# Optimization experiments

Measured on AMD Instinct MI355X. Metric: run time of the kernel, lower is better.

## Reference

```python
import jax, jax.numpy as jnp
import numpy as np

NEG_SLOPE = 0.2  # PyG GATv2Conv default negative_slope


def gatv2_layer(x, src, dst, Wl, bl, Wr, br, att, bias, concat):
    """GATv2Conv (PyG semantics): message j->i, softmax over incoming edges of i."""
    N = x.shape[0]
    H, C = att.shape
    xl = (x @ Wl + bl).reshape(N, H, C)  # source-side transform
    xr = (x @ Wr + br).reshape(N, H, C)  # target-side transform
    msg = xl[src]                                   # [E,H,C] gathered source feats
    e = jax.nn.leaky_relu(msg + xr[dst], NEG_SLOPE)  # [E,H,C]
    score = jnp.einsum('ehc,hc->eh', e, att)        # [E,H]
    # segment softmax over destination node (every node has a self loop -> no empty segment)
    smax = jax.ops.segment_max(score, dst, num_segments=N)
    ex = jnp.exp(score - smax[dst])
    denom = jax.ops.segment_sum(ex, dst, num_segments=N)
    alpha = ex / denom[dst]                         # [E,H]
    out = jax.ops.segment_sum(alpha[:, :, None] * msg, dst, num_segments=N)  # [N,H,C]
    out = out.reshape(N, H * C) if concat else out.mean(axis=1)
    return out + bias


def setup_inputs():
    key = jax.random.key(0)
    ks = jax.random.split(key, 16)
    N, E = 50000, 800000
    D_in, Hd, H, D_out = 128, 32, 4, 64
    HC = Hd * H  # 128
    s = 0.05
    return {
        'x': jax.random.normal(ks[0], (N, D_in), jnp.float32),
        'edge_index': jax.random.randint(ks[1], (2, E), 0, N, dtype=jnp.int32),
        # layer 1: GATv2Conv(D_in, Hd, heads=H)
        'Wl1': jax.random.normal(ks[2], (D_in, HC), jnp.float32) * s,
        'bl1': jnp.zeros((HC,), jnp.float32),
        'Wr1': jax.random.normal(ks[3], (D_in, HC), jnp.float32) * s,
        'br1': jnp.zeros((HC,), jnp.float32),
        'att1': jax.random.normal(ks[4], (H, Hd), jnp.float32) * s,
        'bias1': jnp.zeros((HC,), jnp.float32),
        # layer 2: GATv2Conv(HC, D_out, heads=1, concat=False)
        'Wl2': jax.random.normal(ks[5], (HC, D_out), jnp.float32) * s,
        'bl2': jnp.zeros((D_out,), jnp.float32),
        'Wr2': jax.random.normal(ks[6], (HC, D_out), jnp.float32) * s,
        'br2': jnp.zeros((D_out,), jnp.float32),
        'att2': jax.random.normal(ks[7], (1, D_out), jnp.float32) * s,
        'bias2': jnp.zeros((D_out,), jnp.float32),
    }


def reference(x, edge_index, Wl1, bl1, Wr1, br1, att1, bias1,
              Wl2, bl2, Wr2, br2, att2, bias2):
    N = x.shape[0]
    loops = jnp.arange(N, dtype=edge_index.dtype)  # add_self_loops=True (PyG default)
    src = jnp.concatenate([edge_index[0], loops])
    dst = jnp.concatenate([edge_index[1], loops])
    h = gatv2_layer(x, src, dst, Wl1, bl1, Wr1, br1, att1, bias1, concat=True)
    h = jax.nn.relu(h)
    out = gatv2_layer(h, src, dst, Wl2, bl2, Wr2, br2, att2, bias2, concat=False)
    return out
```

## Files before the change

kernel.cpp:

```cpp
#include <hip/hip_runtime.h>
#include <hip/hip_bf16.h>
#include <math.h>


#define NSLOPE 0.2f
#define L2E 1.4426950408889634f
#define BKT 64
#define POISON 0xAAAAAAAAu

typedef __attribute__((ext_vector_type(8))) short short8;
typedef __attribute__((ext_vector_type(4))) float f32x4;
typedef _Float16 h16x2 __attribute__((ext_vector_type(2)));

__device__ inline unsigned short f2bf(float f) {
  unsigned int u = __float_as_uint(f);
  u += 0x7fff + ((u >> 16) & 1);
  return (unsigned short)(u >> 16);
}
__device__ inline float bf2f(unsigned short h) {
  return __uint_as_float(((unsigned int)h) << 16);
}

__device__ inline float merge2(float qa, float qb, int m, int lane) {
  bool hi = (lane & m) != 0;
  float sel = hi ? qb : qa;
  float oth = hi ? qa : qb;
  return sel + __shfl_xor(oth, m);
}

template <typename AT>
__device__ __forceinline__ void gemm_body(const AT* __restrict__ A,
    const float* __restrict__ Wl, const float* __restrict__ Wr,
    const float* __restrict__ bl, const float* __restrict__ br,
    _Float16* __restrict__ xl, _Float16* __restrict__ xr, int C, int M,
    int mblk, int g, unsigned short* smem) {
  unsigned short* sBh = smem;
  unsigned short* sBl = smem + 8192;
  int t = threadIdx.x;
  for (int s = t; s < 1024; s += 256) {
    int lane = s & 63;
    int kt = (s >> 6) & 3;
    int tn = s >> 8;
    int n = g * 64 + tn * 16 + (lane & 15);
    int k0 = kt * 32 + ((lane >> 4) * 8);
    const float* W = (n < C) ? (Wl + n) : (Wr + (n - C));
    int base = ((tn * 4 + kt) * 64 + lane) * 8;
#pragma unroll
    for (int j = 0; j < 8; j++) {
      float v = W[(size_t)(k0 + j) * C];
      unsigned short hi = f2bf(v);
      sBh[base + j] = hi;
      sBl[base + j] = f2bf(v - bf2f(hi));
    }
  }
  __syncthreads();
  int w = t >> 6, l = t & 63;
  int m_base = mblk * 128 + w * 32;
  int mrow = l & 15;
  int kq = l >> 4;
  f32x4 acc[2][4];
#pragma unroll
  for (int mt = 0; mt < 2; mt++)
#pragma unroll
    for (int tn = 0; tn < 4; tn++) acc[mt][tn] = (f32x4){0.f, 0.f, 0.f, 0.f};

#pragma unroll
  for (int kt = 0; kt < 4; kt++) {
    short8 ah[2], al[2];
#pragma unroll
    for (int mt = 0; mt < 2; mt++) {
      int m = m_base + mt * 16 + mrow;
      m = (m < M) ? m : (M - 1);
      const AT* pa = A + (size_t)m * 128 + kt * 32 + kq * 8;
      float f[8];
      if constexpr (sizeof(AT) == 4) {
        float4 v0 = *(const float4*)pa;
        float4 v1 = *(const float4*)(pa + 4);
        f[0] = v0.x; f[1] = v0.y; f[2] = v0.z; f[3] = v0.w;
        f[4] = v1.x; f[5] = v1.y; f[6] = v1.z; f[7] = v1.w;
      } else {
        h16x2 h0 = *(const h16x2*)(pa + 0);
        h16x2 h1 = *(const h16x2*)(pa + 2);
        h16x2 h2 = *(const h16x2*)(pa + 4);
        h16x2 h3 = *(const h16x2*)(pa + 6);
        f[0] = (float)h0.x; f[1] = (float)h0.y; f[2] = (float)h1.x; f[3] = (float)h1.y;
        f[4] = (float)h2.x; f[5] = (float)h2.y; f[6] = (float)h3.x; f[7] = (float)h3.y;
      }
#pragma unroll
      for (int j = 0; j < 8; j++) {
        unsigned short hi = f2bf(f[j]);
        ah[mt][j] = (short)hi;
        al[mt][j] = (short)f2bf(f[j] - bf2f(hi));
      }
    }
#pragma unroll
    for (int tn = 0; tn < 4; tn++) {
      int off = ((tn * 4 + kt) * 64 + l) * 8;
      short8 bh = *(const short8*)(sBh + off);
      short8 blo = *(const short8*)(sBl + off);
#pragma unroll
      for (int mt = 0; mt < 2; mt++) {
        acc[mt][tn] = __builtin_amdgcn_mfma_f32_16x16x32_bf16(ah[mt], bh, acc[mt][tn], 0, 0, 0);
        acc[mt][tn] = __builtin_amdgcn_mfma_f32_16x16x32_bf16(ah[mt], blo, acc[mt][tn], 0, 0, 0);
        acc[mt][tn] = __builtin_amdgcn_mfma_f32_16x16x32_bf16(al[mt], bh, acc[mt][tn], 0, 0, 0);
      }
    }
  }
  __syncthreads();
  _Float16* stg = (_Float16*)(smem + w * 2304);
#pragma unroll
  for (int tn = 0; tn < 4; tn++) {
    int col = tn * 16 + mrow;
    int bn = g * 64 + col;
    float bias = (bn < C) ? bl[bn] : br[bn - C];
#pragma unroll
    for (int mt = 0; mt < 2; mt++) {
#pragma unroll
      for (int r = 0; r < 4; r++) {
        int row = mt * 16 + kq * 4 + r;
        stg[row * 72 + col] = (_Float16)(acc[mt][tn][r] + bias);
      }
    }
  }
  int gcol = g * 64;
  _Float16* outp = (gcol < C) ? (xl + gcol) : (xr + (gcol - C));
  int row8 = l >> 3, sub = l & 7;
#pragma unroll
  for (int ig = 0; ig < 4; ig++) {
    int row = ig * 8 + row8;
    int m = m_base + row;
    if (m < M) {
      float4 v = *(const float4*)(stg + row * 72 + sub * 8);
      *(float4*)(outp + (size_t)m * C + sub * 8) = v;
    }
  }
}


__global__ __launch_bounds__(256) void fat1_kernel(
    const int* __restrict__ srcv, const int* __restrict__ dstv,
    unsigned int* __restrict__ counts, unsigned short* __restrict__ bucket, int E,
    const float* __restrict__ A,
    const float* __restrict__ Wl, const float* __restrict__ Wr,
    const float* __restrict__ bl, const float* __restrict__ br,
    _Float16* __restrict__ xl, _Float16* __restrict__ xr, int M,
    int countBlocks, int P) {
  __shared__ unsigned short smem[16384];
  int b = blockIdx.x;
  bool isCount = ((b % P) == (P - 1)) && (b / P < countBlocks);
  if (isCount) {
    int cb = b / P;
    int base = cb * 2048 + threadIdx.x;
    int d[8], s[8];
    unsigned r[8];
#pragma unroll
    for (int u = 0; u < 8; u++) {
      int idx = base + u * 256;
      d[u] = (idx < E) ? dstv[idx] : -1;
      s[u] = (idx < E) ? srcv[idx] : 0;
    }
#pragma unroll
    for (int u = 0; u < 8; u++)
      if (d[u] >= 0) r[u] = atomicAdd(&counts[d[u]], 1u) - POISON;
#pragma unroll
    for (int u = 0; u < 8; u++)
      if (d[u] >= 0 && r[u] < BKT) bucket[(size_t)d[u] * BKT + r[u]] = (unsigned short)s[u];
  } else {
    int nbelow = b / P;
    nbelow = nbelow < countBlocks ? nbelow : countBlocks;
    int bid = b - nbelow;
    gemm_body<float>(A, Wl, Wr, bl, br, xl, xr, 128, M, bid >> 2, bid & 3, smem);
  }
}

__global__ __launch_bounds__(256) void gemm2_kernel(const _Float16* __restrict__ A,
    const float* __restrict__ Wl, const float* __restrict__ Wr,
    const float* __restrict__ bl, const float* __restrict__ br,
    _Float16* __restrict__ xl, _Float16* __restrict__ xr, int M) {
  __shared__ unsigned short smem[16384];
  gemm_body<_Float16>(A, Wl, Wr, bl, br, xl, xr, 64, M, blockIdx.x >> 1, blockIdx.x & 1, smem);
}


__device__ inline h16x2 leaky_pk(h16x2 s) {
  h16x2 s2 = s * (h16x2){(_Float16)NSLOPE, (_Float16)NSLOPE};
  return __builtin_elementwise_max(s, s2);
}

__global__ __launch_bounds__(256) void edge1_kernel(
    const _Float16* __restrict__ xl, const _Float16* __restrict__ xr,
    const float* __restrict__ att, const float* __restrict__ bias,
    const unsigned int* __restrict__ counts, const unsigned short* __restrict__ bucket,
    _Float16* __restrict__ h, int N) {
  int node = blockIdx.x * 4 + (threadIdx.x >> 6);
  if (node >= N) return;
  int lane = threadIdx.x & 63;
  int c = lane * 2;
  h16x2 xri = *(const h16x2*)(xr + (size_t)node * 128 + c);
  float2 atf = *(const float2*)(att + c);
  h16x2 at = {(_Float16)(atf.x * L2E), (_Float16)(atf.y * L2E)};
  unsigned dg = counts[node] - POISON;
  int deg = __builtin_amdgcn_readfirstlane((int)(dg < BKT ? dg : BKT));
  const uint4* brow = (const uint4*)(bucket + (size_t)node * BKT);
  int base16 = lane & 48;
  float l, a0, a1;
  {
    h16x2 ms = *(const h16x2*)(xl + (size_t)node * 128 + c);
    h16x2 lk = leaky_pk(ms + xri);
    float q = __builtin_amdgcn_fdot2(lk, at, 0.f, false);
    q += __shfl_xor(q, 1);
    q += __shfl_xor(q, 2);
    q += __shfl_xor(q, 4);
    q += __shfl_xor(q, 8);
    float p = exp2f(q);
    l = p; a0 = p * (float)ms.x; a1 = p * (float)ms.y;
  }
  for (int e = 0; e < deg; e += 8) {
    uint4 pk = brow[e >> 3];
    int j[8];
    j[0] = __builtin_amdgcn_readfirstlane((int)(pk.x & 0xffffu));
    j[1] = __builtin_amdgcn_readfirstlane((int)(pk.x >> 16));
    j[2] = __builtin_amdgcn_readfirstlane((int)(pk.y & 0xffffu));
    j[3] = __builtin_amdgcn_readfirstlane((int)(pk.y >> 16));
    j[4] = __builtin_amdgcn_readfirstlane((int)(pk.z & 0xffffu));
    j[5] = __builtin_amdgcn_readfirstlane((int)(pk.z >> 16));
    j[6] = __builtin_amdgcn_readfirstlane((int)(pk.w & 0xffffu));
    j[7] = __builtin_amdgcn_readfirstlane((int)(pk.w >> 16));
    h16x2 mv[8];
#pragma unroll
    for (int u = 0; u < 8; u++) mv[u] = *(const h16x2*)(xl + (size_t)j[u] * 128 + c);
    float q[8];
#pragma unroll
    for (int u = 0; u < 8; u++) {
      h16x2 lk = leaky_pk(mv[u] + xri);
      q[u] = __builtin_amdgcn_fdot2(lk, at, (e + u < deg) ? 0.f : -1e30f, false);
    }
    float v0 = merge2(q[0], q[1], 1, lane);
    float v1 = merge2(q[2], q[3], 1, lane);
    float v2 = merge2(q[4], q[5], 1, lane);
    float v3 = merge2(q[6], q[7], 1, lane);
    float w0 = merge2(v0, v1, 2, lane);
    float w1 = merge2(v2, v3, 2, lane);
    float uu = merge2(w0, w1, 4, lane);
    uu += __shfl_xor(uu, 8);
    float p = exp2f(uu);
    float cb[8];
#pragma unroll
    for (int u = 0; u < 8; u++) cb[u] = __shfl(p, base16 + u);
#pragma unroll
    for (int u = 0; u < 8; u++) {
      l += cb[u];
      a0 = fmaf(cb[u], (float)mv[u].x, a0);
      a1 = fmaf(cb[u], (float)mv[u].y, a1);
    }
  }
  float inv = 1.f / l;
  float2 bb = *(const float2*)(bias + c);
  float o0 = fmaxf(fmaf(a0, inv, bb.x), 0.f);
  float o1 = fmaxf(fmaf(a1, inv, bb.y), 0.f);
  *(h16x2*)(h + (size_t)node * 128 + c) = (h16x2){(_Float16)o0, (_Float16)o1};
}

__global__ __launch_bounds__(256) void edge2_kernel(
    const _Float16* __restrict__ xl, const _Float16* __restrict__ xr,
    const float* __restrict__ att, const float* __restrict__ bias,
    const unsigned int* __restrict__ counts, const unsigned short* __restrict__ bucket,
    float* __restrict__ out, int N) {
  int node = blockIdx.x * 4 + (threadIdx.x >> 6);
  if (node >= N) return;
  int lane = threadIdx.x & 63;
  int half = lane >> 5;
  int c = (lane & 31) * 2;
  h16x2 xri = *(const h16x2*)(xr + (size_t)node * 64 + c);
  float2 atf = *(const float2*)(att + c);
  h16x2 at = {(_Float16)(atf.x * L2E), (_Float16)(atf.y * L2E)};
  unsigned dg = counts[node] - POISON;
  int deg = __builtin_amdgcn_readfirstlane((int)(dg < BKT ? dg : BKT));
  const uint4* brow = (const uint4*)(bucket + (size_t)node * BKT);
  int hbase = lane & 32;
  float l = 0.f, a0 = 0.f, a1 = 0.f;
  {
    h16x2 ms = *(const h16x2*)(xl + (size_t)node * 64 + c);
    h16x2 lk = leaky_pk(ms + xri);
    float q = __builtin_amdgcn_fdot2(lk, at, 0.f, false);
    q += __shfl_xor(q, 1);
    q += __shfl_xor(q, 2);
    q += __shfl_xor(q, 4);
    q += __shfl_xor(q, 8);
    q += __shfl_xor(q, 16);
    float p = exp2f(q);
    if (half == 0) { l = p; a0 = p * (float)ms.x; a1 = p * (float)ms.y; }
  }
  for (int e = 0; e < deg; e += 8) {
    uint4 pk = brow[e >> 3];
    unsigned wsel[4] = {pk.x, pk.y, pk.z, pk.w};
    int j[4];
#pragma unroll
    for (int u = 0; u < 4; u++)
      j[u] = half ? (int)(wsel[u] >> 16) : (int)(wsel[u] & 0xffffu);
    h16x2 mv[4];
#pragma unroll
    for (int u = 0; u < 4; u++) mv[u] = *(const h16x2*)(xl + (size_t)j[u] * 64 + c);
    float q[4];
#pragma unroll
    for (int u = 0; u < 4; u++) {
      h16x2 lk = leaky_pk(mv[u] + xri);
      q[u] = __builtin_amdgcn_fdot2(lk, at, (e + 2 * u + half < deg) ? 0.f : -1e30f, false);
    }
    float v0 = merge2(q[0], q[1], 1, lane);
    float v1 = merge2(q[2], q[3], 1, lane);
    float uu = merge2(v0, v1, 2, lane);
    uu += __shfl_xor(uu, 4);
    uu += __shfl_xor(uu, 8);
    uu += __shfl_xor(uu, 16);
    float p = exp2f(uu);
    float cb[4];
#pragma unroll
    for (int u = 0; u < 4; u++) cb[u] = __shfl(p, hbase + u);
#pragma unroll
    for (int u = 0; u < 4; u++) {
      l += cb[u];
      a0 = fmaf(cb[u], (float)mv[u].x, a0);
      a1 = fmaf(cb[u], (float)mv[u].y, a1);
    }
  }
  l  += __shfl_xor(l, 32);
  a0 += __shfl_xor(a0, 32);
  a1 += __shfl_xor(a1, 32);
  if (half == 0) {
    float inv = 1.f / l;
    float2 bb = *(const float2*)(bias + c);
    *(float2*)(out + (size_t)node * 64 + c) =
        make_float2(fmaf(a0, inv, bb.x), fmaf(a1, inv, bb.y));
  }
}

extern "C" void kernel_launch(void* const* d_in, const int* in_sizes, int n_in,
                              void* d_out, int out_size, void* d_ws, size_t ws_size,
                              hipStream_t stream) {
  const float* x    = (const float*)d_in[0];
  const int*   ei   = (const int*)d_in[1];
  const float* Wl1  = (const float*)d_in[2];
  const float* bl1  = (const float*)d_in[3];
  const float* Wr1  = (const float*)d_in[4];
  const float* br1  = (const float*)d_in[5];
  const float* att1 = (const float*)d_in[6];
  const float* bias1= (const float*)d_in[7];
  const float* Wl2  = (const float*)d_in[8];
  const float* bl2  = (const float*)d_in[9];
  const float* Wr2  = (const float*)d_in[10];
  const float* br2  = (const float*)d_in[11];
  const float* att2 = (const float*)d_in[12];
  const float* bias2= (const float*)d_in[13];
  float* out = (float*)d_out;

  const int N = in_sizes[0] / 128;
  const int E = in_sizes[1] / 2;
  const int* srcv = ei;
  const int* dstv = ei + E;

  char* ws = (char*)d_ws;
  size_t off = 0;
  auto alloc = [&](size_t bytes) -> void* {
    void* p = ws + off;
    off = (off + bytes + 255) & ~(size_t)255;
    return p;
  };
  unsigned int* counts    = (unsigned int*)alloc((size_t)N * 4);
  unsigned short* bucket  = (unsigned short*)alloc((size_t)N * BKT * 2);
  _Float16* xl1h = (_Float16*)alloc((size_t)N * 128 * 2);
  _Float16* xr1h = (_Float16*)alloc((size_t)N * 128 * 2);
  _Float16* hbuf = (_Float16*)alloc((size_t)N * 128 * 2);
  _Float16* xl2h = xl1h;
  _Float16* xr2h = xr1h;
  (void)ws_size; (void)n_in; (void)out_size;

  int mb = (N + 127) / 128;
  int countBlocks = (E + 2047) / 2048;
  int grid = countBlocks + mb * 4;
  int P = grid / countBlocks;
  if (P < 1) P = 1;

  fat1_kernel<<<grid, 256, 0, stream>>>(
      srcv, dstv, counts, bucket, E, x, Wl1, Wr1, bl1, br1, xl1h, xr1h, N,
      countBlocks, P);
  edge1_kernel<<<(N + 3) / 4, 256, 0, stream>>>(xl1h, xr1h, att1, bias1, counts,
                                                bucket, hbuf, N);
  gemm2_kernel<<<mb * 2, 256, 0, stream>>>(hbuf, Wl2, Wr2, bl2, br2, xl2h, xr2h, N);
  edge2_kernel<<<(N + 3) / 4, 256, 0, stream>>>(xl2h, xr2h, att2, bias2, counts,
                                                bucket, out, N);
}
```

Baseline: 217.9 us.

## Fuse layer-1 edge aggregation with layer-2 GEMM and use fp16 MFMA

The layer-1 edge aggregation now writes each 128-node tile of h into LDS, and the same block immediately runs the layer-2 projection on that tile with MFMA. This removes the hbuf round trip through global memory and one kernel launch. Separately, the split-bf16 three-MFMA emulation of fp32 is replaced by a single fp16 MFMA in both GEMMs. That cuts MFMA work and conversion overhead but lowers precision. The fused kernel launches far fewer blocks (391 instead of 12500), each looping over 32 nodes per wave, which reduces parallelism and latency hiding in the gather phase.

```diff
diff --git a/kernel.cpp b/kernel.cpp
--- a/kernel.cpp
+++ b/kernel.cpp
@@ -8,18 +8,9 @@
 #define BKT 64
 #define POISON 0xAAAAAAAAu
 
-typedef __attribute__((ext_vector_type(8))) short short8;
 typedef __attribute__((ext_vector_type(4))) float f32x4;
 typedef _Float16 h16x2 __attribute__((ext_vector_type(2)));
-
-__device__ inline unsigned short f2bf(float f) {
-  unsigned int u = __float_as_uint(f);
-  u += 0x7fff + ((u >> 16) & 1);
-  return (unsigned short)(u >> 16);
-}
-__device__ inline float bf2f(unsigned short h) {
-  return __uint_as_float(((unsigned int)h) << 16);
-}
+typedef _Float16 half8 __attribute__((ext_vector_type(8)));
 
 __device__ inline float merge2(float qa, float qb, int m, int lane) {
   bool hi = (lane & m) != 0;
@@ -28,14 +19,17 @@
   return sel + __shfl_xor(oth, m);
 }
 
-template <typename AT>
-__device__ __forceinline__ void gemm_body(const AT* __restrict__ A,
+__device__ inline h16x2 leaky_pk(h16x2 s) {
+  h16x2 s2 = s * (h16x2){(_Float16)NSLOPE, (_Float16)NSLOPE};
+  return __builtin_elementwise_max(s, s2);
+}
+
+__device__ __forceinline__ void gemm1_body(const float* __restrict__ A,
     const float* __restrict__ Wl, const float* __restrict__ Wr,
     const float* __restrict__ bl, const float* __restrict__ br,
     _Float16* __restrict__ xl, _Float16* __restrict__ xr, int C, int M,
     int mblk, int g, unsigned short* smem) {
-  unsigned short* sBh = smem;
-  unsigned short* sBl = smem + 8192;
+  _Float16* sB = (_Float16*)smem;
   int t = threadIdx.x;
   for (int s = t; s < 1024; s += 256) {
     int lane = s & 63;
@@ -46,12 +40,7 @@
     const float* W = (n < C) ? (Wl + n) : (Wr + (n - C));
     int base = ((tn * 4 + kt) * 64 + lane) * 8;
 #pragma unroll
-    for (int j = 0; j < 8; j++) {
-      float v = W[(size_t)(k0 + j) * C];
-      unsigned short hi = f2bf(v);
-      sBh[base + j] = hi;
-      sBl[base + j] = f2bf(v - bf2f(hi));
-    }
+    for (int j = 0; j < 8; j++) sB[base + j] = (_Float16)W[(size_t)(k0 + j) * C];
   }
   __syncthreads();
   int w = t >> 6, l = t & 63;
@@ -66,48 +55,26 @@
 
 #pragma unroll
   for (int kt = 0; kt < 4; kt++) {
-    short8 ah[2], al[2];
+    half8 ah[2];
 #pragma unroll
     for (int mt = 0; mt < 2; mt++) {
       int m = m_base + mt * 16 + mrow;
       m = (m < M) ? m : (M - 1);
-      const AT* pa = A + (size_t)m * 128 + kt * 32 + kq * 8;
-      float f[8];
-      if constexpr (sizeof(AT) == 4) {
-        float4 v0 = *(const float4*)pa;
-        float4 v1 = *(const float4*)(pa + 4);
-        f[0] = v0.x; f[1] = v0.y; f[2] = v0.z; f[3] = v0.w;
-        f[4] = v1.x; f[5] = v1.y; f[6] = v1.z; f[7] = v1.w;
-      } else {
-        h16x2 h0 = *(const h16x2*)(pa + 0);
-        h16x2 h1 = *(const h16x2*)(pa + 2);
-        h16x2 h2 = *(const h16x2*)(pa + 4);
-        h16x2 h3 = *(const h16x2*)(pa + 6);
-        f[0] = (float)h0.x; f[1] = (float)h0.y; f[2] = (float)h1.x; f[3] = (float)h1.y;
-        f[4] = (float)h2.x; f[5] = (float)h2.y; f[6] = (float)h3.x; f[7] = (float)h3.y;
-      }
-#pragma unroll
-      for (int j = 0; j < 8; j++) {
-        unsigned short hi = f2bf(f[j]);
-        ah[mt][j] = (short)hi;
-        al[mt][j] = (short)f2bf(f[j] - bf2f(hi));
-      }
+      const float* pa = A + (size_t)m * 128 + kt * 32 + kq * 8;
+      float4 v0 = *(const float4*)pa;
+      float4 v1 = *(const float4*)(pa + 4);
+      ah[mt] = (half8){(_Float16)v0.x, (_Float16)v0.y, (_Float16)v0.z, (_Float16)v0.w,
+                       (_Float16)v1.x, (_Float16)v1.y, (_Float16)v1.z, (_Float16)v1.w};
     }
 #pragma unroll
     for (int tn = 0; tn < 4; tn++) {
-      int off = ((tn * 4 + kt) * 64 + l) * 8;
-      short8 bh = *(const short8*)(sBh + off);
-      short8 blo = *(const short8*)(sBl + off);
-#pragma unroll
-      for (int mt = 0; mt < 2; mt++) {
-        acc[mt][tn] = __builtin_amdgcn_mfma_f32_16x16x32_bf16(ah[mt], bh, acc[mt][tn], 0, 0, 0);
-        acc[mt][tn] = __builtin_amdgcn_mfma_f32_16x16x32_bf16(ah[mt], blo, acc[mt][tn], 0, 0, 0);
-        acc[mt][tn] = __builtin_amdgcn_mfma_f32_16x16x32_bf16(al[mt], bh, acc[mt][tn], 0, 0, 0);
-      }
-    }
-  }
-  __syncthreads();
-  _Float16* stg = (_Float16*)(smem + w * 2304);
+      half8 b = *(const half8*)(sB + ((tn * 4 + kt) * 64 + l) * 8);
+#pragma unroll
+      for (int mt = 0; mt < 2; mt++)
+        acc[mt][tn] = __builtin_amdgcn_mfma_f32_16x16x32_f16(ah[mt], b, acc[mt][tn], 0, 0, 0);
+    }
+  }
+  _Float16* stg = (_Float16*)(smem + 8192) + w * 2304;
 #pragma unroll
   for (int tn = 0; tn < 4; tn++) {
     int col = tn * 16 + mrow;
@@ -145,7 +112,7 @@
     const float* __restrict__ bl, const float* __restrict__ br,
     _Float16* __restrict__ xl, _Float16* __restrict__ xr, int M,
     int countBlocks, int P) {
-  __shared__ unsigned short smem[16384];
+  __shared__ unsigned short smem[17408];
   int b = blockIdx.x;
   bool isCount = ((b % P) == (P - 1)) && (b / P < countBlocks);
   if (isCount) {
@@ -169,97 +136,156 @@
     int nbelow = b / P;
     nbelow = nbelow < countBlocks ? nbelow : countBlocks;
     int bid = b - nbelow;
-    gemm_body<float>(A, Wl, Wr, bl, br, xl, xr, 128, M, bid >> 2, bid & 3, smem);
-  }
-}
-
-__global__ __launch_bounds__(256) void gemm2_kernel(const _Float16* __restrict__ A,
-    const float* __restrict__ Wl, const float* __restrict__ Wr,
-    const float* __restrict__ bl, const float* __restrict__ br,
-    _Float16* __restrict__ xl, _Float16* __restrict__ xr, int M) {
-  __shared__ unsigned short smem[16384];
-  gemm_body<_Float16>(A, Wl, Wr, bl, br, xl, xr, 64, M, blockIdx.x >> 1, blockIdx.x & 1, smem);
-}
-
-
-__device__ inline h16x2 leaky_pk(h16x2 s) {
-  h16x2 s2 = s * (h16x2){(_Float16)NSLOPE, (_Float16)NSLOPE};
-  return __builtin_elementwise_max(s, s2);
-}
-
-__global__ __launch_bounds__(256) void edge1_kernel(
-    const _Float16* __restrict__ xl, const _Float16* __restrict__ xr,
+    gemm1_body(A, Wl, Wr, bl, br, xl, xr, 128, M, bid >> 2, bid & 3, smem);
+  }
+}
+
+__global__ __launch_bounds__(256) void edge1g2_kernel(
+    const _Float16* __restrict__ xl1, const _Float16* __restrict__ xr1,
     const float* __restrict__ att, const float* __restrict__ bias,
     const unsigned int* __restrict__ counts, const unsigned short* __restrict__ bucket,
-    _Float16* __restrict__ h, int N) {
-  int node = blockIdx.x * 4 + (threadIdx.x >> 6);
-  if (node >= N) return;
-  int lane = threadIdx.x & 63;
+    const float* __restrict__ Wl2, const float* __restrict__ Wr2,
+    const float* __restrict__ bl2, const float* __restrict__ br2,
+    _Float16* __restrict__ xl2, _Float16* __restrict__ xr2, int N) {
+  __shared__ _Float16 sh[128 * 136];
+  __shared__ _Float16 sb[9216];
+  int t = threadIdx.x, w = t >> 6, lane = t & 63;
+  int nodeBase = blockIdx.x * 128;
   int c = lane * 2;
-  h16x2 xri = *(const h16x2*)(xr + (size_t)node * 128 + c);
   float2 atf = *(const float2*)(att + c);
   h16x2 at = {(_Float16)(atf.x * L2E), (_Float16)(atf.y * L2E)};
-  unsigned dg = counts[node] - POISON;
-  int deg = __builtin_amdgcn_readfirstlane((int)(dg < BKT ? dg : BKT));
-  const uint4* brow = (const uint4*)(bucket + (size_t)node * BKT);
+  float2 bb = *(const float2*)(bias + c);
   int base16 = lane & 48;
-  float l, a0, a1;
-  {
-    h16x2 ms = *(const h16x2*)(xl + (size_t)node * 128 + c);
-    h16x2 lk = leaky_pk(ms + xri);
-    float q = __builtin_amdgcn_fdot2(lk, at, 0.f, false);
-    q += __shfl_xor(q, 1);
-    q += __shfl_xor(q, 2);
-    q += __shfl_xor(q, 4);
-    q += __shfl_xor(q, 8);
-    float p = exp2f(q);
-    l = p; a0 = p * (float)ms.x; a1 = p * (float)ms.y;
-  }
-  for (int e = 0; e < deg; e += 8) {
-    uint4 pk = brow[e >> 3];
-    int j[8];
-    j[0] = __builtin_amdgcn_readfirstlane((int)(pk.x & 0xffffu));
-    j[1] = __builtin_amdgcn_readfirstlane((int)(pk.x >> 16));
-    j[2] = __builtin_amdgcn_readfirstlane((int)(pk.y & 0xffffu));
-    j[3] = __builtin_amdgcn_readfirstlane((int)(pk.y >> 16));
-    j[4] = __builtin_amdgcn_readfirstlane((int)(pk.z & 0xffffu));
-    j[5] = __builtin_amdgcn_readfirstlane((int)(pk.z >> 16));
-    j[6] = __builtin_amdgcn_readfirstlane((int)(pk.w & 0xffffu));
-    j[7] = __builtin_amdgcn_readfirstlane((int)(pk.w >> 16));
-    h16x2 mv[8];
-#pragma unroll
-    for (int u = 0; u < 8; u++) mv[u] = *(const h16x2*)(xl + (size_t)j[u] * 128 + c);
-    float q[8];
-#pragma unroll
-    for (int u = 0; u < 8; u++) {
-      h16x2 lk = leaky_pk(mv[u] + xri);
-      q[u] = __builtin_amdgcn_fdot2(lk, at, (e + u < deg) ? 0.f : -1e30f, false);
-    }
-    float v0 = merge2(q[0], q[1], 1, lane);
-    float v1 = merge2(q[2], q[3], 1, lane);
-    float v2 = merge2(q[4], q[5], 1, lane);
-    float v3 = merge2(q[6], q[7], 1, lane);
-    float w0 = merge2(v0, v1, 2, lane);
-    float w1 = merge2(v2, v3, 2, lane);
-    float uu = merge2(w0, w1, 4, lane);
-    uu += __shfl_xor(uu, 8);
-    float p = exp2f(uu);
-    float cb[8];
-#pragma unroll
-    for (int u = 0; u < 8; u++) cb[u] = __shfl(p, base16 + u);
-#pragma unroll
-    for (int u = 0; u < 8; u++) {
-      l += cb[u];
-      a0 = fmaf(cb[u], (float)mv[u].x, a0);
-      a1 = fmaf(cb[u], (float)mv[u].y, a1);
-    }
-  }
-  float inv = 1.f / l;
-  float2 bb = *(const float2*)(bias + c);
-  float o0 = fmaxf(fmaf(a0, inv, bb.x), 0.f);
-  float o1 = fmaxf(fmaf(a1, inv, bb.y), 0.f);
-  *(h16x2*)(h + (size_t)node * 128 + c) = (h16x2){(_Float16)o0, (_Float16)o1};
-}
+
+  for (int i = 0; i < 32; i++) {
+    int node = nodeBase + w * 32 + i;
+    if (node >= N) break;
+    h16x2 xri = *(const h16x2*)(xr1 + (size_t)node * 128 + c);
+    unsigned dg = counts[node] - POISON;
+    int deg = __builtin_amdgcn_readfirstlane((int)(dg < BKT ? dg : BKT));
+    const uint4* brow = (const uint4*)(bucket + (size_t)node * BKT);
+    float l, a0, a1;
+    {
+      h16x2 ms = *(const h16x2*)(xl1 + (size_t)node * 128 + c);
+      h16x2 lk = leaky_pk(ms + xri);
+      float q = __builtin_amdgcn_fdot2(lk, at, 0.f, false);
+      q += __shfl_xor(q, 1);
+      q += __shfl_xor(q, 2);
+      q += __shfl_xor(q, 4);
+      q += __shfl_xor(q, 8);
+      float p = exp2f(q);
+      l = p; a0 = p * (float)ms.x; a1 = p * (float)ms.y;
+    }
+    for (int e = 0; e < deg; e += 8) {
+      uint4 pk = brow[e >> 3];
+      int j[8];
+      j[0] = __builtin_amdgcn_readfirstlane((int)(pk.x & 0xffffu));
+      j[1] = __builtin_amdgcn_readfirstlane((int)(pk.x >> 16));
+      j[2] = __builtin_amdgcn_readfirstlane((int)(pk.y & 0xffffu));
+      j[3] = __builtin_amdgcn_readfirstlane((int)(pk.y >> 16));
+      j[4] = __builtin_amdgcn_readfirstlane((int)(pk.z & 0xffffu));
+      j[5] = __builtin_amdgcn_readfirstlane((int)(pk.z >> 16));
+      j[6] = __builtin_amdgcn_readfirstlane((int)(pk.w & 0xffffu));
+      j[7] = __builtin_amdgcn_readfirstlane((int)(pk.w >> 16));
+      h16x2 mv[8];
+#pragma unroll
+      for (int u = 0; u < 8; u++) mv[u] = *(const h16x2*)(xl1 + (size_t)j[u] * 128 + c);
+      float q[8];
+#pragma unroll
+      for (int u = 0; u < 8; u++) {
+        h16x2 lk = leaky_pk(mv[u] + xri);
+        q[u] = __builtin_amdgcn_fdot2(lk, at, (e + u < deg) ? 0.f : -1e30f, false);
+      }
+      float v0 = merge2(q[0], q[1], 1, lane);
+      float v1 = merge2(q[2], q[3], 1, lane);
+      float v2 = merge2(q[4], q[5], 1, lane);
+      float v3 = merge2(q[6], q[7], 1, lane);
+      float w0 = merge2(v0, v1, 2, lane);
+      float w1 = merge2(v2, v3, 2, lane);
+      float uu = merge2(w0, w1, 4, lane);
+      uu += __shfl_xor(uu, 8);
+      float p = exp2f(uu);
+      float cb[8];
+#pragma unroll
+      for (int u = 0; u < 8; u++) cb[u] = __shfl(p, base16 + u);
+#pragma unroll
+      for (int u = 0; u < 8; u++) {
+        l += cb[u];
+        a0 = fmaf(cb[u], (float)mv[u].x, a0);
+        a1 = fmaf(cb[u], (float)mv[u].y, a1);
+      }
+    }
+    float inv = 1.f / l;
+    float o0 = fmaxf(fmaf(a0, inv, bb.x), 0.f);
+    float o1 = fmaxf(fmaf(a1, inv, bb.y), 0.f);
+    *(h16x2*)(sh + (w * 32 + i) * 136 + c) = (h16x2){(_Float16)o0, (_Float16)o1};
+  }
+  __syncthreads();
+
+  int mrow = lane & 15, kq = lane >> 4;
+  for (int g = 0; g < 2; g++) {
+    for (int s = t; s < 1024; s += 256) {
+      int sl = s & 63;
+      int kt = (s >> 6) & 3;
+      int tn = s >> 8;
+      int n = tn * 16 + (sl & 15);
+      int k0 = kt * 32 + ((sl >> 4) * 8);
+      const float* W = (g == 0) ? (Wl2 + n) : (Wr2 + n);
+      int base = ((tn * 4 + kt) * 64 + sl) * 8;
+#pragma unroll
+      for (int j = 0; j < 8; j++) sb[base + j] = (_Float16)W[(size_t)(k0 + j) * 64];
+    }
+    __syncthreads();
+    f32x4 acc[2][4];
+#pragma unroll
+    for (int mt = 0; mt < 2; mt++)
+#pragma unroll
+      for (int tn = 0; tn < 4; tn++) acc[mt][tn] = (f32x4){0.f, 0.f, 0.f, 0.f};
+#pragma unroll
+    for (int kt = 0; kt < 4; kt++) {
+      half8 ah[2];
+#pragma unroll
+      for (int mt = 0; mt < 2; mt++)
+        ah[mt] = *(const half8*)(sh + (w * 32 + mt * 16 + mrow) * 136 + kt * 32 + kq * 8);
+#pragma unroll
+      for (int tn = 0; tn < 4; tn++) {
+        half8 b = *(const half8*)(sb + ((tn * 4 + kt) * 64 + lane) * 8);
+#pragma unroll
+        for (int mt = 0; mt < 2; mt++)
+          acc[mt][tn] = __builtin_amdgcn_mfma_f32_16x16x32_f16(ah[mt], b, acc[mt][tn], 0, 0, 0);
+      }
+    }
+    __syncthreads();
+    _Float16* stg = sb + w * 2304;
+    const float* bv = (g == 0) ? bl2 : br2;
+#pragma unroll
+    for (int tn = 0; tn < 4; tn++) {
+      int col = tn * 16 + mrow;
+      float bias2v = bv[col];
+#pragma unroll
+      for (int mt = 0; mt < 2; mt++) {
+#pragma unroll
+        for (int r = 0; r < 4; r++) {
+          int row = mt * 16 + kq * 4 + r;
+          stg[row * 72 + col] = (_Float16)(acc[mt][tn][r] + bias2v);
+        }
+      }
+    }
+    _Float16* outp = (g == 0) ? xl2 : xr2;
+    int row8 = lane >> 3, sub = lane & 7;
+#pragma unroll
+    for (int ig = 0; ig < 4; ig++) {
+      int row = ig * 8 + row8;
+      int m = nodeBase + w * 32 + row;
+      if (m < N) {
+        float4 v = *(const float4*)(stg + row * 72 + sub * 8);
+        *(float4*)(outp + (size_t)m * 64 + sub * 8) = v;
+      }
+    }
+    __syncthreads();
+  }
+}
+
 
 __global__ __launch_bounds__(256) void edge2_kernel(
     const _Float16* __restrict__ xl, const _Float16* __restrict__ xr,
@@ -329,9 +355,9 @@
   a1 += __shfl_xor(a1, 32);
   if (half == 0) {
     float inv = 1.f / l;
-    float2 bb = *(const float2*)(bias + c);
+    float2 bbv = *(const float2*)(bias + c);
     *(float2*)(out + (size_t)node * 64 + c) =
-        make_float2(fmaf(a0, inv, bb.x), fmaf(a1, inv, bb.y));
+        make_float2(fmaf(a0, inv, bbv.x), fmaf(a1, inv, bbv.y));
   }
 }
 
@@ -370,9 +396,8 @@
   unsigned short* bucket  = (unsigned short*)alloc((size_t)N * BKT * 2);
   _Float16* xl1h = (_Float16*)alloc((size_t)N * 128 * 2);
   _Float16* xr1h = (_Float16*)alloc((size_t)N * 128 * 2);
-  _Float16* hbuf = (_Float16*)alloc((size_t)N * 128 * 2);
-  _Float16* xl2h = xl1h;
-  _Float16* xr2h = xr1h;
+  _Float16* xl2h = (_Float16*)alloc((size_t)N * 64 * 2);
+  _Float16* xr2h = (_Float16*)alloc((size_t)N * 64 * 2);
   (void)ws_size; (void)n_in; (void)out_size;
 
   int mb = (N + 127) / 128;
@@ -384,9 +409,8 @@
   fat1_kernel<<<grid, 256, 0, stream>>>(
       srcv, dstv, counts, bucket, E, x, Wl1, Wr1, bl1, br1, xl1h, xr1h, N,
       countBlocks, P);
-  edge1_kernel<<<(N + 3) / 4, 256, 0, stream>>>(xl1h, xr1h, att1, bias1, counts,
-                                                bucket, hbuf, N);
-  gemm2_kernel<<<mb * 2, 256, 0, stream>>>(hbuf, Wl2, Wr2, bl2, br2, xl2h, xr2h, N);
+  edge1g2_kernel<<<mb, 256, 0, stream>>>(
+      xl1h, xr1h, att1, bias1, counts, bucket, Wl2, Wr2, bl2, br2, xl2h, xr2h, N);
   edge2_kernel<<<(N + 3) / 4, 256, 0, stream>>>(xl2h, xr2h, att2, bias2, counts,
                                                 bucket, out, N);
 }
```

Result: slower. 280.1 us (+28.5%).
